# Optimization experiments

Hardware: AMD Instinct MI355X
Metric: run time of the kernel (lower is better)

The kernel has to match this reference:

```python
import jax, jax.numpy as jnp
import numpy as np

N_NODES = 100000
N_EDGES = 1600000
D_IN = 128
D_HID = 128
D_OUT = 64


def spmm(vals, row, col, x):
    # sparse [N,N] @ dense [N,D]: out[r] = sum_e vals[e] * x[col[e]] for row[e]==r
    msgs = vals[:, None] * x[col]            # [E, D]
    return jax.ops.segment_sum(msgs, row, num_segments=N_NODES)


def setup_inputs() -> dict:
    key = jax.random.key(0)
    ks = jax.random.split(key, 8)
    x = jax.random.normal(ks[0], (N_NODES, D_IN), dtype=jnp.float32)
    vals = jax.random.uniform(ks[1], (N_EDGES,), dtype=jnp.float32)
    W1 = jax.random.normal(ks[2], (D_IN, D_HID), dtype=jnp.float32) * (1.0 / np.sqrt(D_IN))
    b1 = jnp.zeros((D_HID,), dtype=jnp.float32)
    W2 = jax.random.normal(ks[3], (D_HID, D_HID), dtype=jnp.float32) * (1.0 / np.sqrt(D_HID))
    b2 = jnp.zeros((D_HID,), dtype=jnp.float32)
    W3 = jax.random.normal(ks[4], (D_HID, D_OUT), dtype=jnp.float32) * (1.0 / np.sqrt(D_HID))
    b3 = jnp.zeros((D_OUT,), dtype=jnp.float32)
    row = jax.random.randint(ks[5], (N_EDGES,), 0, N_NODES, dtype=jnp.int32)
    col = jax.random.randint(ks[6], (N_EDGES,), 0, N_NODES, dtype=jnp.int32)
    return {"x": x, "vals": vals, "W1": W1, "b1": b1, "W2": W2, "b2": b2,
            "W3": W3, "b3": b3, "row": row, "col": col}


def reference(x, vals, W1, b1, W2, b2, W3, b3, row, col):
    # GCNConv 1: linear -> spmm -> relu
    h = jax.nn.relu(spmm(vals, row, col, x @ W1 + b1))
    # GCNConv 2: linear -> spmm -> relu
    h = jax.nn.relu(spmm(vals, row, col, h @ W2 + b2))
    # GCNConv 3 (output): linear -> spmm, no activation
    out = spmm(vals, row, col, h @ W3 + b3)
    return out
```

## Files before the change

kernel.cpp:

```cpp
#include <hip/hip_runtime.h>

#define N_NODES 100000
#define N_EDGES 1600000

#define NBK 782
#define EPB 8192
#define NBA 196
#define CAPE 4096

typedef __attribute__((ext_vector_type(8))) short short8;
typedef __attribute__((ext_vector_type(4))) float f32x4;

__device__ __forceinline__ ushort f2bf(float f) {
    uint u = __float_as_uint(f);
    return (ushort)((u + 0x7fff + ((u >> 16) & 1)) >> 16);
}
__device__ __forceinline__ float bflo(uint p) { return __uint_as_float(p << 16); }
__device__ __forceinline__ float bfhi(uint p) { return __uint_as_float(p & 0xffff0000u); }


__global__ void __launch_bounds__(1024) binA_k(const int* __restrict__ row,
                                               const int* __restrict__ col,
                                               const float* __restrict__ vals,
                                               int2* __restrict__ tmp,
                                               int* __restrict__ offT) {
    __shared__ int cnt[NBK];
    __shared__ int exo[NBK];
    __shared__ int wpart[16];
    int t = threadIdx.x;
    int lane = t & 63;
    int base = blockIdx.x * EPB;

    int rr[8], cc[8], rk[8];
    float vv[8];
#pragma unroll
    for (int u = 0; u < 8; ++u) {
        int e = base + u * 1024 + t;
        bool ok = (e < N_EDGES);
        rr[u] = ok ? row[e] : -1;
        cc[u] = ok ? col[e] : 0;
        vv[u] = ok ? vals[e] : 0.f;
    }

    if (t < NBK) cnt[t] = 0;
    __syncthreads();
#pragma unroll
    for (int u = 0; u < 8; ++u)
        if (rr[u] >= 0) rk[u] = atomicAdd(&cnt[rr[u] >> 7], 1);
    __syncthreads();
    int hv = (t < NBK) ? cnt[t] : 0;

    int v = hv;
    for (int off = 1; off < 64; off <<= 1) {
        int u2 = __shfl_up(v, off);
        if (lane >= off) v += u2;
    }
    if (lane == 63) wpart[t >> 6] = v;
    __syncthreads();
    if (t == 0) {
        int acc = 0;
#pragma unroll
        for (int i = 0; i < 16; ++i) { int w = wpart[i]; wpart[i] = acc; acc += w; }
    }
    __syncthreads();
    v += wpart[t >> 6];
    if (t < NBK) {
        int ex = v - hv;
        exo[t] = ex;
        offT[t * NBA + blockIdx.x] = ex;
    }
    if (t == NBK - 1) offT[NBK * NBA + blockIdx.x] = v;
    __syncthreads();
#pragma unroll
    for (int u = 0; u < 8; ++u) {
        if (rr[u] >= 0) {
            int p = exo[rr[u] >> 7] + rk[u];
            int2 w;
            w.x = ((rr[u] & 127) << 17) | cc[u];
            w.y = __float_as_int(vv[u]);
            tmp[base + p] = w;
        }
    }
}


__device__ void binB_body(int b, const int2* __restrict__ tmp,
                          const int* __restrict__ offT, int* __restrict__ rowptr,
                          int2* __restrict__ ep) {
    __shared__ int goff[NBA];
    __shared__ int scnt[NBA];
    __shared__ int sdst[NBA];
    __shared__ int h[128];
    __shared__ int cur[128];
    __shared__ int2 ebuf[CAPE];
    __shared__ int wpart[4];
    __shared__ int wq[4];
    __shared__ int hp;
    int t = threadIdx.x;
    int lane = t & 63;

    int o0 = 0, c = 0;
    if (t < NBA) {
        o0 = offT[b * NBA + t];
        int o1 = offT[(b + 1) * NBA + t];
        c = o1 - o0;
        goff[t] = t * EPB + o0;
        scnt[t] = c;
    }
    int part = o0;
#pragma unroll
    for (int off = 1; off < 64; off <<= 1) part += __shfl_xor(part, off);
    if (lane == 0) wq[t >> 6] = part;
    if (b == 0 && t == 0) rowptr[N_NODES] = N_EDGES;

    int v = c;
    for (int off = 1; off < 64; off <<= 1) {
        int u = __shfl_up(v, off);
        if (lane >= off) v += u;
    }
    if (lane == 63) wpart[t >> 6] = v;
    if (t < 128) h[t] = 0;
    __syncthreads();
    if (t == 0) {
        int acc = 0;
#pragma unroll
        for (int i = 0; i < 4; ++i) { int w = wpart[i]; wpart[i] = acc; acc += w; }
    }
    __syncthreads();
    v += wpart[t >> 6];
    if (t < NBA) sdst[t] = v - c;
    __syncthreads();

    int grp = t >> 4, gl = t & 15;
    for (int s = grp; s < NBA; s += 16) {
        int n = scnt[s], go = goff[s], dd = sdst[s];
        for (int i = gl; i < n; i += 16) {
            int2 e = tmp[go + i];
            atomicAdd(&h[e.x >> 17], 1);
            ebuf[dd + i] = e;
        }
    }
    __syncthreads();
    int hv = (t < 128) ? h[t] : 0;
    int sv = hv;
    for (int off = 1; off < 64; off <<= 1) {
        int u = __shfl_up(sv, off);
        if (lane >= off) sv += u;
    }
    if (t == 63) hp = sv;
    __syncthreads();
    int bs = wq[0] + wq[1] + wq[2] + wq[3];
    if (t < 128) {
        int inc = sv + ((t >= 64) ? hp : 0);
        int ex = inc - hv;
        cur[t] = ex;
        int r = (b << 7) + t;
        if (r < N_NODES) rowptr[r] = bs + ex;
    }
    __syncthreads();
    int T = sdst[NBA - 1] + scnt[NBA - 1];
    for (int j = t; j < T; j += 256) {
        int2 e = ebuf[j];
        int p = atomicAdd(&cur[e.x >> 17], 1);
        int2 w;
        w.x = e.x & 0x1ffff;
        w.y = e.y;
        ep[bs + p] = w;
    }
}


__device__ void gemm1_body(int bid, const float* __restrict__ Xf,
                           const ushort* __restrict__ Wt,
                           const float* __restrict__ bias, ushort* __restrict__ Y) {
    int wv = threadIdx.x >> 6;
    int l = threadIdx.x & 63;
    int lg = l >> 4, lm = l & 15;
    int rbase = bid * 64 + wv * 16;

    int arow = rbase + lm;
    if (arow > N_NODES - 1) arow = N_NODES - 1;

    f32x4 acc[8];
#pragma unroll
    for (int n = 0; n < 8; n++) acc[n] = (f32x4){0.f, 0.f, 0.f, 0.f};

#pragma unroll
    for (int kk = 0; kk < 4; ++kk) {
        const float* ap = Xf + (size_t)arow * 128 + kk * 32 + lg * 8;
        float4 u = *(const float4*)ap;
        float4 v = *(const float4*)(ap + 4);
        short8 a = (short8){(short)f2bf(u.x), (short)f2bf(u.y), (short)f2bf(u.z),
                            (short)f2bf(u.w), (short)f2bf(v.x), (short)f2bf(v.y),
                            (short)f2bf(v.z), (short)f2bf(v.w)};
#pragma unroll
        for (int n = 0; n < 8; ++n) {
            short8 b = *(const short8*)(Wt + (size_t)(n * 16 + lm) * 128 + kk * 32 + lg * 8);
            acc[n] = __builtin_amdgcn_mfma_f32_16x16x32_bf16(a, b, acc[n], 0, 0, 0);
        }
    }

    int r0 = rbase + lg * 4;
#pragma unroll
    for (int n = 0; n < 8; ++n) {
        int c = n * 16 + lm;
        float bj = bias[c];
#pragma unroll
        for (int i = 0; i < 4; ++i) {
            int r = r0 + i;
            if (r < N_NODES) Y[(size_t)r * 128 + c] = f2bf(acc[n][i] + bj);
        }
    }
}

__global__ void __launch_bounds__(256) fusedB_k(const int2* __restrict__ tmp,
                                                const int* __restrict__ offT,
                                                int* __restrict__ rowptr,
                                                int2* __restrict__ ep,
                                                const float* __restrict__ x,
                                                const ushort* __restrict__ Wt1,
                                                const float* __restrict__ b1,
                                                ushort* __restrict__ g) {
    if (blockIdx.x < NBK)
        binB_body(blockIdx.x, tmp, offT, rowptr, ep);
    else
        gemm1_body(blockIdx.x - NBK, x, Wt1, b1, g);
}


__global__ void wcvt_k(const float* __restrict__ W1, const float* __restrict__ W2,
                       const float* __restrict__ W3, ushort* __restrict__ Wt1,
                       ushort* __restrict__ Wt2, ushort* __restrict__ Wt3) {
    int i = blockIdx.x * 256 + threadIdx.x;
    if (i < 16384) {
        int n = i >> 7, k = i & 127;
        Wt1[i] = f2bf(W1[k * 128 + n]);
        Wt2[i] = f2bf(W2[k * 128 + n]);
    }
    if (i < 8192) {
        int n = i >> 7, k = i & 127;
        Wt3[i] = f2bf(W3[k * 64 + n]);
    }
}


template <int DN>
__global__ void __launch_bounds__(256) gemm_k(const ushort* __restrict__ Xb,
                                              const ushort* __restrict__ Wt,
                                              const float* __restrict__ bias,
                                              ushort* __restrict__ Y) {
    constexpr int NT = DN / 16;
    int wv = threadIdx.x >> 6;
    int l = threadIdx.x & 63;
    int lg = l >> 4, lm = l & 15;
    int rbase = blockIdx.x * 64 + wv * 16;

    int arow = rbase + lm;
    if (arow > N_NODES - 1) arow = N_NODES - 1;

    f32x4 acc[NT];
#pragma unroll
    for (int n = 0; n < NT; n++) acc[n] = (f32x4){0.f, 0.f, 0.f, 0.f};

#pragma unroll
    for (int kk = 0; kk < 4; ++kk) {
        short8 a = *(const short8*)(Xb + (size_t)arow * 128 + kk * 32 + lg * 8);
#pragma unroll
        for (int n = 0; n < NT; ++n) {
            short8 b = *(const short8*)(Wt + (size_t)(n * 16 + lm) * 128 + kk * 32 + lg * 8);
            acc[n] = __builtin_amdgcn_mfma_f32_16x16x32_bf16(a, b, acc[n], 0, 0, 0);
        }
    }

    int r0 = rbase + lg * 4;
#pragma unroll
    for (int n = 0; n < NT; ++n) {
        int c = n * 16 + lm;
        float bj = bias[c];
#pragma unroll
        for (int i = 0; i < 4; ++i) {
            int r = r0 + i;
            if (r < N_NODES) Y[(size_t)r * DN + c] = f2bf(acc[n][i] + bj);
        }
    }
}


#define SPMM_BODY(EPREAD)                                                     \
    if (D == 128) {                                                           \
        const uint4* xp = (const uint4*)xb;                                   \
        float a0 = 0.f, a1 = 0.f, a2 = 0.f, a3 = 0.f;                         \
        float a4 = 0.f, a5 = 0.f, a6 = 0.f, a7 = 0.f;                         \
        int i = s;                                                            \
        for (; i + 4 <= e; i += 4) {                                          \
            int2 e0 = EPREAD(i), e1 = EPREAD(i + 1);                          \
            int2 e2 = EPREAD(i + 2), e3 = EPREAD(i + 3);                      \
            uint4 x0 = xp[e0.x * 16 + hl];                                    \
            uint4 x1 = xp[e1.x * 16 + hl];                                    \
            uint4 x2 = xp[e2.x * 16 + hl];                                    \
            uint4 x3 = xp[e3.x * 16 + hl];                                    \
            float v0 = __int_as_float(e0.y), v1 = __int_as_float(e1.y);       \
            float v2 = __int_as_float(e2.y), v3 = __int_as_float(e3.y);       \
            a0 = fmaf(v0, bflo(x0.x), a0); a1 = fmaf(v0, bfhi(x0.x), a1);     \
            a2 = fmaf(v0, bflo(x0.y), a2); a3 = fmaf(v0, bfhi(x0.y), a3);     \
            a4 = fmaf(v0, bflo(x0.z), a4); a5 = fmaf(v0, bfhi(x0.z), a5);     \
            a6 = fmaf(v0, bflo(x0.w), a6); a7 = fmaf(v0, bfhi(x0.w), a7);     \
            a0 = fmaf(v1, bflo(x1.x), a0); a1 = fmaf(v1, bfhi(x1.x), a1);     \
            a2 = fmaf(v1, bflo(x1.y), a2); a3 = fmaf(v1, bfhi(x1.y), a3);     \
            a4 = fmaf(v1, bflo(x1.z), a4); a5 = fmaf(v1, bfhi(x1.z), a5);     \
            a6 = fmaf(v1, bflo(x1.w), a6); a7 = fmaf(v1, bfhi(x1.w), a7);     \
            a0 = fmaf(v2, bflo(x2.x), a0); a1 = fmaf(v2, bfhi(x2.x), a1);     \
            a2 = fmaf(v2, bflo(x2.y), a2); a3 = fmaf(v2, bfhi(x2.y), a3);     \
            a4 = fmaf(v2, bflo(x2.z), a4); a5 = fmaf(v2, bfhi(x2.z), a5);     \
            a6 = fmaf(v2, bflo(x2.w), a6); a7 = fmaf(v2, bfhi(x2.w), a7);     \
            a0 = fmaf(v3, bflo(x3.x), a0); a1 = fmaf(v3, bfhi(x3.x), a1);     \
            a2 = fmaf(v3, bflo(x3.y), a2); a3 = fmaf(v3, bfhi(x3.y), a3);     \
            a4 = fmaf(v3, bflo(x3.z), a4); a5 = fmaf(v3, bfhi(x3.z), a5);     \
            a6 = fmaf(v3, bflo(x3.w), a6); a7 = fmaf(v3, bfhi(x3.w), a7);     \
        }                                                                     \
        for (; i < e; ++i) {                                                  \
            int2 e0 = EPREAD(i);                                              \
            uint4 x0 = xp[e0.x * 16 + hl];                                    \
            float v0 = __int_as_float(e0.y);                                  \
            a0 = fmaf(v0, bflo(x0.x), a0); a1 = fmaf(v0, bfhi(x0.x), a1);     \
            a2 = fmaf(v0, bflo(x0.y), a2); a3 = fmaf(v0, bfhi(x0.y), a3);     \
            a4 = fmaf(v0, bflo(x0.z), a4); a5 = fmaf(v0, bfhi(x0.z), a5);     \
            a6 = fmaf(v0, bflo(x0.w), a6); a7 = fmaf(v0, bfhi(x0.w), a7);     \
        }                                                                     \
        if (RELU) {                                                           \
            a0 = fmaxf(a0, 0.f); a1 = fmaxf(a1, 0.f);                         \
            a2 = fmaxf(a2, 0.f); a3 = fmaxf(a3, 0.f);                         \
            a4 = fmaxf(a4, 0.f); a5 = fmaxf(a5, 0.f);                         \
            a6 = fmaxf(a6, 0.f); a7 = fmaxf(a7, 0.f);                         \
        }                                                                     \
        uint4 o;                                                              \
        o.x = (uint)f2bf(a0) | ((uint)f2bf(a1) << 16);                        \
        o.y = (uint)f2bf(a2) | ((uint)f2bf(a3) << 16);                        \
        o.z = (uint)f2bf(a4) | ((uint)f2bf(a5) << 16);                        \
        o.w = (uint)f2bf(a6) | ((uint)f2bf(a7) << 16);                        \
        ((uint4*)y)[w * 16 + hl] = o;                                         \
    } else {                                                                  \
        const uint2* xp = (const uint2*)xb;                                   \
        float a0 = 0.f, a1 = 0.f, a2 = 0.f, a3 = 0.f;                         \
        int i = s;                                                            \
        for (; i + 4 <= e; i += 4) {                                          \
            int2 e0 = EPREAD(i), e1 = EPREAD(i + 1);                          \
            int2 e2 = EPREAD(i + 2), e3 = EPREAD(i + 3);                      \
            uint2 x0 = xp[e0.x * 16 + hl];                                    \
            uint2 x1 = xp[e1.x * 16 + hl];                                    \
            uint2 x2 = xp[e2.x * 16 + hl];                                    \
            uint2 x3 = xp[e3.x * 16 + hl];                                    \
            float v0 = __int_as_float(e0.y), v1 = __int_as_float(e1.y);       \
            float v2 = __int_as_float(e2.y), v3 = __int_as_float(e3.y);       \
            a0 = fmaf(v0, bflo(x0.x), a0); a1 = fmaf(v0, bfhi(x0.x), a1);     \
            a2 = fmaf(v0, bflo(x0.y), a2); a3 = fmaf(v0, bfhi(x0.y), a3);     \
            a0 = fmaf(v1, bflo(x1.x), a0); a1 = fmaf(v1, bfhi(x1.x), a1);     \
            a2 = fmaf(v1, bflo(x1.y), a2); a3 = fmaf(v1, bfhi(x1.y), a3);     \
            a0 = fmaf(v2, bflo(x2.x), a0); a1 = fmaf(v2, bfhi(x2.x), a1);     \
            a2 = fmaf(v2, bflo(x2.y), a2); a3 = fmaf(v2, bfhi(x2.y), a3);     \
            a0 = fmaf(v3, bflo(x3.x), a0); a1 = fmaf(v3, bfhi(x3.x), a1);     \
            a2 = fmaf(v3, bflo(x3.y), a2); a3 = fmaf(v3, bfhi(x3.y), a3);     \
        }                                                                     \
        for (; i < e; ++i) {                                                  \
            int2 e0 = EPREAD(i);                                              \
            uint2 x0 = xp[e0.x * 16 + hl];                                    \
            float v0 = __int_as_float(e0.y);                                  \
            a0 = fmaf(v0, bflo(x0.x), a0); a1 = fmaf(v0, bfhi(x0.x), a1);     \
            a2 = fmaf(v0, bflo(x0.y), a2); a3 = fmaf(v0, bfhi(x0.y), a3);     \
        }                                                                     \
        if (RELU) {                                                           \
            a0 = fmaxf(a0, 0.f); a1 = fmaxf(a1, 0.f);                         \
            a2 = fmaxf(a2, 0.f); a3 = fmaxf(a3, 0.f);                         \
        }                                                                     \
        float4 o; o.x = a0; o.y = a1; o.z = a2; o.w = a3;                     \
        ((float4*)y)[w * 16 + hl] = o;                                        \
    }

template <int D, bool RELU>
__global__ void __launch_bounds__(256) spmm_k(const int* __restrict__ rowptr,
                                              const int2* __restrict__ ep,
                                              const ushort* __restrict__ xb,
                                              void* __restrict__ y) {
    constexpr int CAP = 1536;
    __shared__ int2 eb[CAP];
    __shared__ int sh_s0, sh_n;
    int t = threadIdx.x;
    int g = t >> 4, hl = t & 15;
    int rbase = blockIdx.x * 16;
    int w = rbase + g;

    if (t == 0) {
        int s0 = rowptr[rbase];
        int rend = rbase + 16; if (rend > N_NODES) rend = N_NODES;
        sh_s0 = s0;
        sh_n = rowptr[rend] - s0;
    }
    __syncthreads();
    int s0 = sh_s0, n = sh_n;
    bool inlds = (n <= CAP);
    if (inlds) {
        for (int j = t; j < n; j += 256) eb[j] = ep[s0 + j];
    }
    __syncthreads();
    if (w >= N_NODES) return;
    int s = rowptr[w], e = rowptr[w + 1];

    if (inlds) {
        s -= s0; e -= s0;
#define EPL(i) eb[i]
        SPMM_BODY(EPL)
#undef EPL
    } else {
#define EPG(i) ep[i]
        SPMM_BODY(EPG)
#undef EPG
    }
}


extern "C" void kernel_launch(void* const* d_in, const int* in_sizes, int n_in,
                              void* d_out, int out_size, void* d_ws, size_t ws_size,
                              hipStream_t stream) {
    const float* x    = (const float*)d_in[0];
    const float* vals = (const float*)d_in[1];
    const float* W1   = (const float*)d_in[2];
    const float* b1   = (const float*)d_in[3];
    const float* W2   = (const float*)d_in[4];
    const float* b2   = (const float*)d_in[5];
    const float* W3   = (const float*)d_in[6];
    const float* b3   = (const float*)d_in[7];
    const int* row    = (const int*)d_in[8];
    const int* col    = (const int*)d_in[9];
    float* out = (float*)d_out;

    char* ws = (char*)d_ws;
    int2*   ep     = (int2*)  (ws + 0);
    int*    rowptr = (int*)   (ws + 12800000);
    ushort* Wt1    = (ushort*)(ws + 13601024);
    ushort* Wt2    = (ushort*)(ws + 13633792);
    ushort* Wt3    = (ushort*)(ws + 13666560);
    int*    offT   = (int*)   (ws + 13700096);
    ushort* g64    = (ushort*)(ws + 16000000);
    ushort* g      = (ushort*)(ws + 41600000);
    ushort* sbuf   = (ushort*)(ws + 67200000);

    int2* tmp = (int2*)sbuf;

    hipLaunchKernelGGL(wcvt_k, dim3(64), dim3(256), 0, stream,
                       W1, W2, W3, Wt1, Wt2, Wt3);

    hipLaunchKernelGGL(binA_k, dim3(NBA), dim3(1024), 0, stream,
                       row, col, vals, tmp, offT);

    const int GEMM_GRID = (N_NODES + 63) / 64;
    const int SPMM_GRID = (N_NODES + 15) / 16;

    hipLaunchKernelGGL(fusedB_k, dim3(NBK + GEMM_GRID), dim3(256), 0, stream,
                       tmp, offT, rowptr, ep, x, Wt1, b1, g);

    hipLaunchKernelGGL((spmm_k<128, true>), dim3(SPMM_GRID), dim3(256), 0, stream,
                       rowptr, ep, g, sbuf);
    hipLaunchKernelGGL((gemm_k<128>), dim3(GEMM_GRID), dim3(256), 0, stream, sbuf, Wt2, b2, g);
    hipLaunchKernelGGL((spmm_k<128, true>), dim3(SPMM_GRID), dim3(256), 0, stream,
                       rowptr, ep, g, sbuf);
    hipLaunchKernelGGL((gemm_k<64>), dim3(GEMM_GRID), dim3(256), 0, stream, sbuf, Wt3, b3, g64);
    hipLaunchKernelGGL((spmm_k<64, false>), dim3(SPMM_GRID), dim3(256), 0, stream,
                       rowptr, ep, g64, out);
}
```

Baseline: 290.0 us.

## Fuse SpMM aggregation with following dense GEMM via LDS staging

Layer-2 and layer-3 linear transforms are fused into the preceding SpMM kernel. Each block aggregates 16 rows, applies ReLU, stages the bf16 result in padded LDS, then runs MFMA against the weight matrix and writes the next layer's pre-aggregation features. This removes two kernel launches and one full write and read of the intermediate activation buffer. In exchange it adds a block barrier and LDS use per block, plus a GEMM tail in each SpMM block, and relies on N_NODES being divisible by 16.

```diff
diff --git a/kernel.cpp b/kernel.cpp
--- a/kernel.cpp
+++ b/kernel.cpp
@@ -244,50 +244,8 @@
 }
 
 
-template <int DN>
-__global__ void __launch_bounds__(256) gemm_k(const ushort* __restrict__ Xb,
-                                              const ushort* __restrict__ Wt,
-                                              const float* __restrict__ bias,
-                                              ushort* __restrict__ Y) {
-    constexpr int NT = DN / 16;
-    int wv = threadIdx.x >> 6;
-    int l = threadIdx.x & 63;
-    int lg = l >> 4, lm = l & 15;
-    int rbase = blockIdx.x * 64 + wv * 16;
-
-    int arow = rbase + lm;
-    if (arow > N_NODES - 1) arow = N_NODES - 1;
-
-    f32x4 acc[NT];
-#pragma unroll
-    for (int n = 0; n < NT; n++) acc[n] = (f32x4){0.f, 0.f, 0.f, 0.f};
-
-#pragma unroll
-    for (int kk = 0; kk < 4; ++kk) {
-        short8 a = *(const short8*)(Xb + (size_t)arow * 128 + kk * 32 + lg * 8);
-#pragma unroll
-        for (int n = 0; n < NT; ++n) {
-            short8 b = *(const short8*)(Wt + (size_t)(n * 16 + lm) * 128 + kk * 32 + lg * 8);
-            acc[n] = __builtin_amdgcn_mfma_f32_16x16x32_bf16(a, b, acc[n], 0, 0, 0);
-        }
-    }
-
-    int r0 = rbase + lg * 4;
-#pragma unroll
-    for (int n = 0; n < NT; ++n) {
-        int c = n * 16 + lm;
-        float bj = bias[c];
-#pragma unroll
-        for (int i = 0; i < 4; ++i) {
-            int r = r0 + i;
-            if (r < N_NODES) Y[(size_t)r * DN + c] = f2bf(acc[n][i] + bj);
-        }
-    }
-}
-
-
-#define SPMM_BODY(EPREAD)                                                     \
-    if (D == 128) {                                                           \
+#define SPMMG_P1(EPREAD)                                                      \
+    {                                                                         \
         const uint4* xp = (const uint4*)xb;                                   \
         float a0 = 0.f, a1 = 0.f, a2 = 0.f, a3 = 0.f;                         \
         float a4 = 0.f, a5 = 0.f, a6 = 0.f, a7 = 0.f;                         \
@@ -327,21 +285,117 @@
             a4 = fmaf(v0, bflo(x0.z), a4); a5 = fmaf(v0, bfhi(x0.z), a5);     \
             a6 = fmaf(v0, bflo(x0.w), a6); a7 = fmaf(v0, bfhi(x0.w), a7);     \
         }                                                                     \
-        if (RELU) {                                                           \
-            a0 = fmaxf(a0, 0.f); a1 = fmaxf(a1, 0.f);                         \
-            a2 = fmaxf(a2, 0.f); a3 = fmaxf(a3, 0.f);                         \
-            a4 = fmaxf(a4, 0.f); a5 = fmaxf(a5, 0.f);                         \
-            a6 = fmaxf(a6, 0.f); a7 = fmaxf(a7, 0.f);                         \
-        }                                                                     \
+        a0 = fmaxf(a0, 0.f); a1 = fmaxf(a1, 0.f);                             \
+        a2 = fmaxf(a2, 0.f); a3 = fmaxf(a3, 0.f);                             \
+        a4 = fmaxf(a4, 0.f); a5 = fmaxf(a5, 0.f);                             \
+        a6 = fmaxf(a6, 0.f); a7 = fmaxf(a7, 0.f);                             \
         uint4 o;                                                              \
         o.x = (uint)f2bf(a0) | ((uint)f2bf(a1) << 16);                        \
         o.y = (uint)f2bf(a2) | ((uint)f2bf(a3) << 16);                        \
         o.z = (uint)f2bf(a4) | ((uint)f2bf(a5) << 16);                        \
         o.w = (uint)f2bf(a6) | ((uint)f2bf(a7) << 16);                        \
-        ((uint4*)y)[w * 16 + hl] = o;                                         \
-    } else {                                                                  \
-        const uint2* xp = (const uint2*)xb;                                   \
-        float a0 = 0.f, a1 = 0.f, a2 = 0.f, a3 = 0.f;                         \
+        xl4[g * 17 + hl] = o;                                                 \
+    }
+
+template <int DNO>
+__global__ void __launch_bounds__(256) spmmg_k(const int* __restrict__ rowptr,
+                                               const int2* __restrict__ ep,
+                                               const ushort* __restrict__ xb,
+                                               const ushort* __restrict__ Wt,
+                                               const float* __restrict__ bias,
+                                               ushort* __restrict__ Y) {
+    constexpr int CAP = 1536;
+    __shared__ int2 eb[CAP];
+    __shared__ uint4 xl4[16 * 17];
+    __shared__ int sh_s0, sh_n;
+    int t = threadIdx.x;
+    int g = t >> 4, hl = t & 15;
+    int rbase = blockIdx.x * 16;
+
+    if (t == 0) {
+        int s0 = rowptr[rbase];
+        sh_s0 = s0;
+        sh_n = rowptr[rbase + 16] - s0;
+    }
+    __syncthreads();
+    int s0 = sh_s0, n = sh_n;
+    bool inlds = (n <= CAP);
+    if (inlds) {
+        for (int j = t; j < n; j += 256) eb[j] = ep[s0 + j];
+    }
+    __syncthreads();
+    int s = rowptr[rbase + g], e = rowptr[rbase + g + 1];
+
+    if (inlds) {
+        s -= s0; e -= s0;
+#define EPL(i) eb[i]
+        SPMMG_P1(EPL)
+#undef EPL
+    } else {
+#define EPG(i) ep[i]
+        SPMMG_P1(EPG)
+#undef EPG
+    }
+    __syncthreads();
+
+    constexpr int TPW = DNO / 64;
+    const ushort* xl = (const ushort*)xl4;
+    int wv = t >> 6;
+    int l = t & 63;
+    int lg = l >> 4, lm = l & 15;
+#pragma unroll
+    for (int tt = 0; tt < TPW; ++tt) {
+        int ct = wv * TPW + tt;
+        f32x4 acc = (f32x4){0.f, 0.f, 0.f, 0.f};
+#pragma unroll
+        for (int kk = 0; kk < 4; ++kk) {
+            short8 a = *(const short8*)(xl + lm * 136 + kk * 32 + lg * 8);
+            short8 b = *(const short8*)(Wt + (size_t)(ct * 16 + lm) * 128 + kk * 32 + lg * 8);
+            acc = __builtin_amdgcn_mfma_f32_16x16x32_bf16(a, b, acc, 0, 0, 0);
+        }
+        int c = ct * 16 + lm;
+        float bj = bias[c];
+        int r0 = rbase + lg * 4;
+#pragma unroll
+        for (int i = 0; i < 4; ++i) {
+            int r = r0 + i;
+            if (r < N_NODES) Y[(size_t)r * DNO + c] = f2bf(acc[i] + bj);
+        }
+    }
+}
+
+
+__global__ void __launch_bounds__(256) spmm64_k(const int* __restrict__ rowptr,
+                                                const int2* __restrict__ ep,
+                                                const ushort* __restrict__ xb,
+                                                float* __restrict__ y) {
+    constexpr int CAP = 1536;
+    __shared__ int2 eb[CAP];
+    __shared__ int sh_s0, sh_n;
+    int t = threadIdx.x;
+    int g = t >> 4, hl = t & 15;
+    int rbase = blockIdx.x * 16;
+    int w = rbase + g;
+
+    if (t == 0) {
+        int s0 = rowptr[rbase];
+        sh_s0 = s0;
+        sh_n = rowptr[rbase + 16] - s0;
+    }
+    __syncthreads();
+    int s0 = sh_s0, n = sh_n;
+    bool inlds = (n <= CAP);
+    if (inlds) {
+        for (int j = t; j < n; j += 256) eb[j] = ep[s0 + j];
+    }
+    __syncthreads();
+    int s = rowptr[w], e = rowptr[w + 1];
+
+    const uint2* xp = (const uint2*)xb;
+    float a0 = 0.f, a1 = 0.f, a2 = 0.f, a3 = 0.f;
+
+#define S64_BODY(EPREAD)                                                      \
+    {                                                                         \
         int i = s;                                                            \
         for (; i + 4 <= e; i += 4) {                                          \
             int2 e0 = EPREAD(i), e1 = EPREAD(i + 1);                          \
@@ -368,53 +422,21 @@
             a0 = fmaf(v0, bflo(x0.x), a0); a1 = fmaf(v0, bfhi(x0.x), a1);     \
             a2 = fmaf(v0, bflo(x0.y), a2); a3 = fmaf(v0, bfhi(x0.y), a3);     \
         }                                                                     \
-        if (RELU) {                                                           \
-            a0 = fmaxf(a0, 0.f); a1 = fmaxf(a1, 0.f);                         \
-            a2 = fmaxf(a2, 0.f); a3 = fmaxf(a3, 0.f);                         \
-        }                                                                     \
-        float4 o; o.x = a0; o.y = a1; o.z = a2; o.w = a3;                     \
-        ((float4*)y)[w * 16 + hl] = o;                                        \
-    }
-
-template <int D, bool RELU>
-__global__ void __launch_bounds__(256) spmm_k(const int* __restrict__ rowptr,
-                                              const int2* __restrict__ ep,
-                                              const ushort* __restrict__ xb,
-                                              void* __restrict__ y) {
-    constexpr int CAP = 1536;
-    __shared__ int2 eb[CAP];
-    __shared__ int sh_s0, sh_n;
-    int t = threadIdx.x;
-    int g = t >> 4, hl = t & 15;
-    int rbase = blockIdx.x * 16;
-    int w = rbase + g;
-
-    if (t == 0) {
-        int s0 = rowptr[rbase];
-        int rend = rbase + 16; if (rend > N_NODES) rend = N_NODES;
-        sh_s0 = s0;
-        sh_n = rowptr[rend] - s0;
-    }
-    __syncthreads();
-    int s0 = sh_s0, n = sh_n;
-    bool inlds = (n <= CAP);
-    if (inlds) {
-        for (int j = t; j < n; j += 256) eb[j] = ep[s0 + j];
-    }
-    __syncthreads();
-    if (w >= N_NODES) return;
-    int s = rowptr[w], e = rowptr[w + 1];
+    }
 
     if (inlds) {
         s -= s0; e -= s0;
 #define EPL(i) eb[i]
-        SPMM_BODY(EPL)
+        S64_BODY(EPL)
 #undef EPL
     } else {
 #define EPG(i) ep[i]
-        SPMM_BODY(EPG)
+        S64_BODY(EPG)
 #undef EPG
     }
+#undef S64_BODY
+    float4 o; o.x = a0; o.y = a1; o.z = a2; o.w = a3;
+    ((float4*)y)[w * 16 + hl] = o;
 }
 
 
@@ -453,17 +475,15 @@
                        row, col, vals, tmp, offT);
 
     const int GEMM_GRID = (N_NODES + 63) / 64;
-    const int SPMM_GRID = (N_NODES + 15) / 16;
+    const int SPMM_GRID = N_NODES / 16;
 
     hipLaunchKernelGGL(fusedB_k, dim3(NBK + GEMM_GRID), dim3(256), 0, stream,
                        tmp, offT, rowptr, ep, x, Wt1, b1, g);
 
-    hipLaunchKernelGGL((spmm_k<128, true>), dim3(SPMM_GRID), dim3(256), 0, stream,
-                       rowptr, ep, g, sbuf);
-    hipLaunchKernelGGL((gemm_k<128>), dim3(GEMM_GRID), dim3(256), 0, stream, sbuf, Wt2, b2, g);
-    hipLaunchKernelGGL((spmm_k<128, true>), dim3(SPMM_GRID), dim3(256), 0, stream,
-                       rowptr, ep, g, sbuf);
-    hipLaunchKernelGGL((gemm_k<64>), dim3(GEMM_GRID), dim3(256), 0, stream, sbuf, Wt3, b3, g64);
-    hipLaunchKernelGGL((spmm_k<64, false>), dim3(SPMM_GRID), dim3(256), 0, stream,
+    hipLaunchKernelGGL((spmmg_k<128>), dim3(SPMM_GRID), dim3(256), 0, stream,
+                       rowptr, ep, g, Wt2, b2, sbuf);
+    hipLaunchKernelGGL((spmmg_k<64>), dim3(SPMM_GRID), dim3(256), 0, stream,
+                       rowptr, ep, sbuf, Wt3, b3, g64);
+    hipLaunchKernelGGL(spmm64_k, dim3(SPMM_GRID), dim3(256), 0, stream,
                        rowptr, ep, g64, out);
 }
```

Measured after the change: 244.3 us. -15.8%, faster.
